# Kernel optimization log

Hardware: AMD Instinct MI355X
Metric: run time of the kernel (lower is better)

The kernel has to match this reference:

```python
import jax, jax.numpy as jnp
import numpy as np

N = 8192
H = 256
E = N * 32
ALPHA = 0.2  # LeakyReLU negative slope from init kwarg alpha


def setup_inputs() -> dict:
    key = jax.random.key(0)
    ks = jax.random.split(key, 8)
    s = 1.0 / np.sqrt(H)
    return {
        "features": jax.random.normal(ks[0], (N, H), jnp.float32),
        "edge_index": jax.random.randint(ks[1], (2, E), 0, N, jnp.int64),
        "W_att": jax.random.normal(ks[2], (H, H), jnp.float32) * s,
        "a_src": jax.random.normal(ks[3], (H,), jnp.float32) * s,
        "a_dst": jax.random.normal(ks[4], (H,), jnp.float32) * s,
        "gcn_w": jax.random.normal(ks[5], (H, H), jnp.float32) * s,
        "gcn_b": jnp.zeros((H,), jnp.float32),
        "out_w": jax.random.normal(ks[6], (H, 2), jnp.float32) * s,
        "out_b": jnp.zeros((2,), jnp.float32),
    }


def reference(features, edge_index, W_att, a_src, a_dst, gcn_w, gcn_b, out_w, out_b):
    n = features.shape[0]
    # --- SingleNodeAttentionLayer (GAT-style dense self-attention, concat=True) ---
    Wh = features @ W_att                       # [N, H]
    e = jax.nn.leaky_relu(
        (Wh @ a_src)[:, None] + (Wh @ a_dst)[None, :], negative_slope=ALPHA
    )                                            # [N, N]
    attn = jax.nn.softmax(e, axis=-1)
    h1 = jax.nn.elu(attn @ Wh)                   # [N, H]
    # --- GCNConv: symmetric-normalized aggregation with self-loops ---
    loops = jnp.arange(n, dtype=edge_index.dtype)
    row = jnp.concatenate([edge_index[0], loops])  # destination
    col = jnp.concatenate([edge_index[1], loops])  # source
    deg = jax.ops.segment_sum(jnp.ones_like(row, dtype=h1.dtype), row, num_segments=n)
    dinv = jax.lax.rsqrt(jnp.maximum(deg, 1e-12))
    norm = dinv[row] * dinv[col]                 # [E+N]
    x = h1 @ gcn_w                               # [N, H]
    agg = jax.ops.segment_sum(x[col] * norm[:, None], row, num_segments=n) + gcn_b
    # --- head: linear -> mean over nodes -> softmax ---
    res = agg @ out_w + out_b                    # [N, 2]
    res = jnp.mean(res, axis=0, keepdims=True)   # [1, 2]
    return jax.nn.softmax(res, axis=-1)
```

## Files before the change

### kernel.cpp

```cpp
#include <hip/hip_runtime.h>
#include <hip/hip_bf16.h>

#define NN 8192
#define HH 256
#define EE (NN*32)
#define ALPHAC 0.2f
#define CHUNK 16
#define NCHUNK (NN/CHUNK)
#define CSPAD 1024

typedef __bf16 bf16x8 __attribute__((ext_vector_type(8)));
typedef __bf16 bf16x4v __attribute__((ext_vector_type(4)));
typedef float  f32x4  __attribute__((ext_vector_type(4)));

#define OFF_WH     0
#define OFF_S      (OFF_WH + NN*HH)
#define OFF_SORTD  (OFF_S + NN)
#define OFF_PERM   (OFF_SORTD + NN)
#define OFF_EA     (OFF_PERM + NN)
#define OFF_E1     (OFF_EA + NN)
#define OFF_SAREL  (OFF_E1 + NN)
#define OFF_SBREL  (OFF_SAREL + NN)
#define OFF_ABPART (OFF_SBREL + NN)
#define OFF_CPAB   (OFF_ABPART + 2*NN*HH)
#define OFF_CSA    (OFF_CPAB + 2*(NCHUNK+1)*HH)
#define OFF_CSB    (OFF_CSA + CSPAD)
#define OFF_DEG    (OFF_CSB + CSPAD)
#define OFF_V      (OFF_DEG + NN)
#define OFF_WNODE  (OFF_V + HH)
#define OFF_KEYS   (OFF_WNODE + NN)
#define OFF_CTR    (OFF_KEYS + 2*NN)

__device__ __forceinline__ float elu1(float x) {
    return x > 0.f ? x : (expf(x) - 1.f);
}

__global__ __launch_bounds__(256) void k_main(
        const float* __restrict__ features, const int* __restrict__ ei,
        const float* __restrict__ W_att, const float* __restrict__ a_src,
        const float* __restrict__ a_dst, float* ws) {
    __shared__ __bf16 As[64*264];
    __shared__ __bf16 Bs[64*264];
    __shared__ float wsld[256], wdld[256];
    int bid = blockIdx.x, tid = threadIdx.x;
    if (bid < 512) {
        int mt = bid >> 2, nt = bid & 3;
        int row0 = mt*64, n0 = nt*64;
        if (nt == 0) {
            float accs = 0.f, accd = 0.f;
            const float* wrow = W_att + (size_t)tid*HH;
            #pragma unroll 4
            for (int n = 0; n < HH; n += 4) {
                float4 wv = *(const float4*)(wrow + n);
                float4 av = *(const float4*)(a_src + n);
                float4 dv = *(const float4*)(a_dst + n);
                accs += wv.x*av.x + wv.y*av.y + wv.z*av.z + wv.w*av.w;
                accd += wv.x*dv.x + wv.y*dv.y + wv.z*dv.z + wv.w*dv.w;
            }
            wsld[tid] = accs; wdld[tid] = accd;
        }
        #pragma unroll
        for (int q = 0; q < 16; ++q) {
            int idx = q*256 + tid;
            int rr = idx >> 6, cc = (idx & 63)*4;
            float4 vv = *(const float4*)(features + (size_t)(row0+rr)*HH + cc);
            bf16x4v pv = {(__bf16)vv.x, (__bf16)vv.y, (__bf16)vv.z, (__bf16)vv.w};
            *(bf16x4v*)&As[rr*264 + cc] = pv;
        }
        int nn_ = tid & 63, kb = tid >> 6;
        #pragma unroll 8
        for (int kk = 0; kk < 256; kk += 4)
            Bs[nn_*264 + kk + kb] = (__bf16)W_att[(size_t)(kk + kb)*HH + n0 + nn_];
        __syncthreads();
        int wave = tid >> 6, lane = tid & 63;
        int ml = lane & 15, quad = lane >> 4;
        const __bf16* Ap = &As[(wave*16 + ml)*264 + quad*8];
        const __bf16* Bp = &Bs[ml*264 + quad*8];
        f32x4 ac0 = {0.f,0.f,0.f,0.f}, ac1 = ac0, ac2 = ac0, ac3 = ac0;
        #pragma unroll
        for (int k0 = 0; k0 < HH; k0 += 32) {
            bf16x8 af = *(const bf16x8*)(Ap + k0);
            ac0 = __builtin_amdgcn_mfma_f32_16x16x32_bf16(af, *(const bf16x8*)(Bp + k0), ac0, 0, 0, 0);
            ac1 = __builtin_amdgcn_mfma_f32_16x16x32_bf16(af, *(const bf16x8*)(Bp + 16*264 + k0), ac1, 0, 0, 0);
            ac2 = __builtin_amdgcn_mfma_f32_16x16x32_bf16(af, *(const bf16x8*)(Bp + 32*264 + k0), ac2, 0, 0, 0);
            ac3 = __builtin_amdgcn_mfma_f32_16x16x32_bf16(af, *(const bf16x8*)(Bp + 48*264 + k0), ac3, 0, 0, 0);
        }
        float* Whp = ws + OFF_WH;
        int orow = row0 + wave*16 + quad*4;
        #pragma unroll
        for (int r = 0; r < 4; ++r) {
            size_t g = (size_t)(orow + r)*HH + n0 + ml;
            Whp[g +  0] = ac0[r];
            Whp[g + 16] = ac1[r];
            Whp[g + 32] = ac2[r];
            Whp[g + 48] = ac3[r];
        }
        if (nt == 0) {
            float4 wsv = *(const float4*)&wsld[lane*4];
            float4 wdv = *(const float4*)&wdld[lane*4];
            for (int r = 0; r < 16; ++r) {
                int row = row0 + wave*16 + r;
                bf16x4v av = *(const bf16x4v*)&As[(wave*16+r)*264 + lane*4];
                float a0 = (float)av[0], a1 = (float)av[1], a2 = (float)av[2], a3 = (float)av[3];
                float ss = a0*wsv.x + a1*wsv.y + a2*wsv.z + a3*wsv.w;
                float dd = a0*wdv.x + a1*wdv.y + a2*wdv.z + a3*wdv.w;
                #pragma unroll
                for (int off = 32; off; off >>= 1) {
                    ss += __shfl_xor(ss, off);
                    dd += __shfl_xor(dd, off);
                }
                if (lane == 0) {
                    ws[OFF_S + row] = ss;
                    unsigned u = __float_as_uint(dd);
                    unsigned mono = u ^ ((u & 0x80000000u) ? 0xFFFFFFFFu : 0x80000000u);
                    ((unsigned long long*)(ws + OFF_KEYS))[row] =
                        (((unsigned long long)mono) << 13) | (unsigned)row;
                }
            }
        }
    } else {
        if (bid == 512 && tid == 0) {
            unsigned* ctr = (unsigned*)(ws + OFF_CTR);
            __hip_atomic_store(&ctr[0], 0u, __ATOMIC_RELAXED, __HIP_MEMORY_SCOPE_AGENT);
            __hip_atomic_store(&ctr[1], 0u, __ATOMIC_RELAXED, __HIP_MEMORY_SCOPE_AGENT);
        }
        int e0 = (bid - 512)*512 + tid;
        atomicAdd(ws + OFF_DEG + ei[e0], 1.0f);
        atomicAdd(ws + OFF_DEG + ei[e0+256], 1.0f);
    }
}

__global__ __launch_bounds__(256) void k_rank(const int* __restrict__ ei, float* ws) {
    __shared__ unsigned long long lk[NN];
    int bid = blockIdx.x, tid = threadIdx.x;
    if (bid < 512) {
        const unsigned long long* keys = (const unsigned long long*)(ws + OFF_KEYS);
        for (int m = tid; m < NN/2; m += 256)
            *(ulonglong2*)&lk[m*2] = *(const ulonglong2*)&keys[m*2];
        __syncthreads();
        int wave = tid >> 6, lane = tid & 63;
        int jb = bid*16 + wave*4;
        unsigned long long kj0 = lk[jb+0], kj1 = lk[jb+1];
        unsigned long long kj2 = lk[jb+2], kj3 = lk[jb+3];
        int c0 = 0, c1 = 0, c2 = 0, c3 = 0;
        #pragma unroll 4
        for (int it = 0; it < 64; ++it) {
            ulonglong2 kq = *(const ulonglong2*)&lk[(it*64 + lane)*2];
            c0 += (kq.x < kj0); c1 += (kq.x < kj1);
            c2 += (kq.x < kj2); c3 += (kq.x < kj3);
            c0 += (kq.y < kj0); c1 += (kq.y < kj1);
            c2 += (kq.y < kj2); c3 += (kq.y < kj3);
        }
        #pragma unroll
        for (int off = 1; off < 64; off <<= 1) {
            c0 += __shfl_xor(c0, off);
            c1 += __shfl_xor(c1, off);
            c2 += __shfl_xor(c2, off);
            c3 += __shfl_xor(c3, off);
        }
        if (lane == 0) {
            unsigned long long kk[4] = {kj0, kj1, kj2, kj3};
            int cr[4] = {c0, c1, c2, c3};
            #pragma unroll
            for (int q = 0; q < 4; ++q) {
                unsigned long long kv = kk[q];
                int r = cr[q];
                unsigned mm = (unsigned)(kv >> 13);
                unsigned u = (mm & 0x80000000u) ? (mm ^ 0x80000000u) : ~mm;
                float dj = __uint_as_float(u);
                int j = (int)(kv & 8191ULL);
                ws[OFF_SORTD + r] = dj;
                ((int*)ws)[OFF_PERM + r] = j;
                ws[OFF_EA + r] = expf(ALPHAC * dj);
                ws[OFF_E1 + r] = expf(dj);
            }
        }
    } else {
        int e0 = (bid - 512)*512 + tid;
        #pragma unroll
        for (int q = 0; q < 2; ++q) {
            int e = e0 + q*256;
            int r = ei[e], c = ei[EE + e];
            float dr = rsqrtf(ws[OFF_DEG + r] + 1.0f);
            float dc = rsqrtf(ws[OFF_DEG + c] + 1.0f);
            atomicAdd(ws + OFF_WNODE + c, dr*dc);
        }
    }
}

__global__ __launch_bounds__(256) void k_vecpref(float* ws) {
    __shared__ int   sp[CHUNK];
    __shared__ float sea[CHUNK], se1[CHUNK];
    __shared__ int srank;
    int bid = blockIdx.x, tid = threadIdx.x;
    int c = bid, h = tid;
    int k0 = c * CHUNK;
    unsigned* ctr = (unsigned*)(ws + OFF_CTR);
    if (h < CHUNK) {
        sp[h]  = ((int*)ws)[OFF_PERM + k0 + h];
        sea[h] = ws[OFF_EA + k0 + h];
        se1[h] = ws[OFF_E1 + k0 + h];
    }
    __syncthreads();
    if (tid < 64) {
        float vv = 0.f;
        if (tid < 16) vv = sea[tid];
        else if (tid < 32) vv = se1[tid-16];
        #pragma unroll
        for (int off = 1; off < 16; off <<= 1) {
            float x = __shfl_up(vv, off);
            if ((tid & 15) >= off) vv += x;
        }
        if (tid < 16) {
            ws[OFF_SAREL + k0 + tid] = vv;
            if (tid == 15)
                __hip_atomic_store(&ws[OFF_CSA + c + 1], vv, __ATOMIC_RELAXED, __HIP_MEMORY_SCOPE_AGENT);
        } else if (tid < 32) {
            ws[OFF_SBREL + k0 + tid - 16] = vv;
            if (tid == 31)
                __hip_atomic_store(&ws[OFF_CSB + c + 1], vv, __ATOMIC_RELAXED, __HIP_MEMORY_SCOPE_AGENT);
        }
    }
    const float* Wh = ws + OFF_WH;
    float wv[CHUNK];
    #pragma unroll
    for (int kk = 0; kk < CHUNK; ++kk)
        wv[kk] = Wh[(size_t)sp[kk]*HH + h];
    float2* abp = (float2*)(ws + OFF_ABPART);
    float acca = 0.f, accb = 0.f;
    #pragma unroll
    for (int kk = 0; kk < CHUNK; ++kk) {
        acca += sea[kk]*wv[kk]; accb += se1[kk]*wv[kk];
        abp[(size_t)(k0+kk)*HH + h] = make_float2(acca, accb);
    }
    float2 tot = make_float2(acca, accb);
    unsigned long long totbits;
    __builtin_memcpy(&totbits, &tot, 8);
    float2* cp = (float2*)(ws + OFF_CPAB);
    __hip_atomic_store((unsigned long long*)&cp[(size_t)(c+1)*HH + h], totbits,
                       __ATOMIC_RELAXED, __HIP_MEMORY_SCOPE_AGENT);
    __syncthreads();
    if (tid == 0) {
        unsigned old = __hip_atomic_fetch_add(&ctr[0], 1u, __ATOMIC_RELAXED, __HIP_MEMORY_SCOPE_AGENT);
        srank = (int)old;
    }
    __syncthreads();
    int rk = srank;
    if (rk < NCHUNK - 33) return;
    if (tid == 0) {
        while (__hip_atomic_load(&ctr[0], __ATOMIC_RELAXED, __HIP_MEMORY_SCOPE_AGENT) != (unsigned)NCHUNK)
            __builtin_amdgcn_s_sleep(8);
    }
    __syncthreads();
    int sid = rk - (NCHUNK - 33);
    if (sid < 32) {
        int hh = sid*8 + (tid >> 5);
        int t = tid & 31;
        float la[16], lb[16];
        float ta = 0.f, tb = 0.f;
        #pragma unroll
        for (int m = 0; m < 16; ++m) {
            unsigned long long u = __hip_atomic_load(
                (unsigned long long*)&cp[(size_t)(t*16 + m + 1)*HH + hh],
                __ATOMIC_RELAXED, __HIP_MEMORY_SCOPE_AGENT);
            float2 v; __builtin_memcpy(&v, &u, 8);
            la[m] = v.x; lb[m] = v.y;
            ta += la[m]; tb += lb[m];
        }
        float ia = ta, ib = tb;
        #pragma unroll
        for (int off = 1; off < 32; off <<= 1) {
            float xa = __shfl_up(ia, off, 32);
            float xb = __shfl_up(ib, off, 32);
            if (t >= off) { ia += xa; ib += xb; }
        }
        float ba = ia - ta, bb = ib - tb;
        #pragma unroll
        for (int m = 0; m < 16; ++m) {
            cp[(size_t)(t*16 + m)*HH + hh] = make_float2(ba, bb);
            ba += la[m]; bb += lb[m];
        }
        if (t == 31) cp[(size_t)NCHUNK*HH + hh] = make_float2(ba, bb);
    } else {
        int wv_ = tid >> 6, ln = tid & 63;
        if (wv_ < 2) {
            float* cs = ws + (wv_ ? OFF_CSB : OFF_CSA);
            float la[8];
            float ta = 0.f;
            #pragma unroll
            for (int m = 0; m < 8; ++m) {
                la[m] = __hip_atomic_load(&cs[ln*8 + m + 1], __ATOMIC_RELAXED, __HIP_MEMORY_SCOPE_AGENT);
                ta += la[m];
            }
            float ia = ta;
            #pragma unroll
            for (int off = 1; off < 64; off <<= 1) {
                float x = __shfl_up(ia, off);
                if (ln >= off) ia += x;
            }
            float ba = ia - ta;
            #pragma unroll
            for (int m = 0; m < 8; ++m) { cs[ln*8 + m] = ba; ba += la[m]; }
            if (ln == 63) cs[NCHUNK] = ba;
        }
    }
}

__global__ __launch_bounds__(256) void k_rows(const float* __restrict__ gcn_w,
                                              const float* __restrict__ gcn_b,
                                              const float* __restrict__ out_w,
                                              const float* __restrict__ out_b,
                                              float* ws, float* out) {
    __shared__ float sd[NN];
    __shared__ float red[4][256];
    __shared__ int lastf;
    int bid = blockIdx.x, tid = threadIdx.x;
    unsigned* ctr = (unsigned*)(ws + OFF_CTR);
    for (int m = tid; m < NN/4; m += 256)
        *(float4*)&sd[m*4] = *(const float4*)(ws + OFF_SORTD + m*4);
    __syncthreads();
    int wave = tid >> 6, lane = tid & 63;
    int gw = bid*4 + wave;
    const float2* abp  = (const float2*)(ws + OFF_ABPART);
    const float2* cpab = (const float2*)(ws + OFF_CPAB);
    float btot = ws[OFF_CSB + NCHUNK];
    const float4* btr = (const float4*)(cpab + (size_t)NCHUNK*HH);
    float4 bt0 = btr[lane*2], bt1 = btr[lane*2+1];
    float BTx = bt0.y, BTy = bt0.w, BTz = bt1.y, BTw = bt1.w;

    int myr = lane & 3;
    float si_m = ws[OFF_S + gw*4 + myr];
    float tt = -si_m;
    int lo = 0, hi = NN;
    while (lo < hi) {
        int mid = (lo + hi) >> 1;
        if (sd[mid] <= tt) lo = mid + 1; else hi = mid;
    }
    float accx = 0.f, accy = 0.f, accz = 0.f, accw = 0.f;
    #pragma unroll
    for (int r = 0; r < 4; ++r) {
        int i = gw*4 + r;
        int k = __shfl(lo, r);
        float si = __shfl(si_m, r);
        float eas = expf(ALPHAC * si), es = expf(si);
        float av = 0.f, bv = 0.f;
        float Ax=0.f, Ay=0.f, Az=0.f, Aw=0.f, Bx=0.f, By=0.f, Bz=0.f, Bw=0.f;
        if (k > 0) {
            int km = k - 1, cc = km >> 4;
            av = ws[OFF_CSA + cc] + ws[OFF_SAREL + km];
            bv = ws[OFF_CSB + cc] + ws[OFF_SBREL + km];
            const float4* pr = (const float4*)(abp + (size_t)km*HH);
            const float4* cr = (const float4*)(cpab + (size_t)cc*HH);
            float4 p0 = pr[lane*2], p1 = pr[lane*2+1];
            float4 q0 = cr[lane*2], q1 = cr[lane*2+1];
            Ax = p0.x + q0.x; Bx = p0.y + q0.y;
            Ay = p0.z + q0.z; By = p0.w + q0.w;
            Az = p1.x + q1.x; Bz = p1.y + q1.y;
            Aw = p1.z + q1.z; Bw = p1.w + q1.w;
        }
        float Z = eas*av + es*(btot - bv);
        float invZ = 1.f / Z;
        float w = ws[OFF_WNODE + i] + 1.0f/(ws[OFF_DEG + i] + 1.0f);
        accx += w * elu1((eas*Ax + es*(BTx - Bx)) * invZ);
        accy += w * elu1((eas*Ay + es*(BTy - By)) * invZ);
        accz += w * elu1((eas*Az + es*(BTz - Bz)) * invZ);
        accw += w * elu1((eas*Aw + es*(BTw - Bw)) * invZ);
    }
    red[wave][lane*4+0] = accx;
    red[wave][lane*4+1] = accy;
    red[wave][lane*4+2] = accz;
    red[wave][lane*4+3] = accw;
    __syncthreads();
    float sum = red[0][tid] + red[1][tid] + red[2][tid] + red[3][tid];
    atomicAdd(ws + OFF_V + tid, sum);
    __syncthreads();
    if (tid == 0) {
        unsigned old = __hip_atomic_fetch_add(&ctr[1], 1u, __ATOMIC_RELAXED, __HIP_MEMORY_SCOPE_AGENT);
        lastf = (old == 511u);
    }
    __syncthreads();
    if (!lastf) return;
    float vt = atomicAdd(ws + OFF_V + tid, 0.0f);
    red[0][tid] = vt;
    __syncthreads();
    float acc = 0.f;
    for (int hh = 0; hh < HH; ++hh) acc += red[0][hh] * gcn_w[(size_t)hh*HH + tid];
    float meanv = acc * (1.0f/(float)NN) + gcn_b[tid];
    red[1][tid] = meanv * out_w[tid*2+0];
    red[2][tid] = meanv * out_w[tid*2+1];
    __syncthreads();
    for (int off = 128; off; off >>= 1) {
        if (tid < off) { red[1][tid] += red[1][tid+off]; red[2][tid] += red[2][tid+off]; }
        __syncthreads();
    }
    if (tid == 0) {
        float res0 = red[1][0] + out_b[0], res1 = red[2][0] + out_b[1];
        float m = fmaxf(res0, res1);
        float e0 = expf(res0 - m), e1v = expf(res1 - m);
        float inv = 1.f / (e0 + e1v);
        out[0] = e0 * inv;
        out[1] = e1v * inv;
    }
}

extern "C" void kernel_launch(void* const* d_in, const int* in_sizes, int n_in,
                              void* d_out, int out_size, void* d_ws, size_t ws_size,
                              hipStream_t stream) {
    const float* features = (const float*)d_in[0];
    const int*   eidx     = (const int*)d_in[1];
    const float* W_att    = (const float*)d_in[2];
    const float* a_src    = (const float*)d_in[3];
    const float* a_dst    = (const float*)d_in[4];
    const float* gcn_w    = (const float*)d_in[5];
    const float* gcn_b    = (const float*)d_in[6];
    const float* out_w    = (const float*)d_in[7];
    const float* out_b    = (const float*)d_in[8];
    float* ws  = (float*)d_ws;
    float* out = (float*)d_out;

    k_main<<<1024, 256, 0, stream>>>(features, eidx, W_att, a_src, a_dst, ws);
    k_rank<<<1024, 256, 0, stream>>>(eidx, ws);
    k_vecpref<<<NCHUNK, 256, 0, stream>>>(ws);
    k_rows<<<512, 256, 0, stream>>>(gcn_w, gcn_b, out_w, out_b, ws, out);
}
```

Before: 181.3 us.

## Fuse attention score projections into GEMM epilogue and merge edge work into GEMM blocks

The attention scores s and d are now computed from the MFMA accumulators in the GEMM epilogue, using shuffle reductions plus atomicAdd into workspace. This replaces the separate W·a precompute and the per-row dot products. The degree-count and edge-weight atomics now run inside the same 512 blocks as the GEMM and rank work, which halves both grids. Rank keys are built in shared memory straight from d, the exp tables move into k_vecpref, and k_rows binary-searches global sorted d instead of staging it in LDS. The atomics assume the workspace starts zeroed, and the global-memory binary search may add latency.

```diff
diff --git a/kernel.cpp b/kernel.cpp
--- a/kernel.cpp
+++ b/kernel.cpp
@@ -15,11 +15,10 @@
 
 #define OFF_WH     0
 #define OFF_S      (OFF_WH + NN*HH)
-#define OFF_SORTD  (OFF_S + NN)
+#define OFF_D      (OFF_S + NN)
+#define OFF_SORTD  (OFF_D + NN)
 #define OFF_PERM   (OFF_SORTD + NN)
-#define OFF_EA     (OFF_PERM + NN)
-#define OFF_E1     (OFF_EA + NN)
-#define OFF_SAREL  (OFF_E1 + NN)
+#define OFF_SAREL  (OFF_PERM + NN)
 #define OFF_SBREL  (OFF_SAREL + NN)
 #define OFF_ABPART (OFF_SBREL + NN)
 #define OFF_CPAB   (OFF_ABPART + 2*NN*HH)
@@ -28,8 +27,7 @@
 #define OFF_DEG    (OFF_CSB + CSPAD)
 #define OFF_V      (OFF_DEG + NN)
 #define OFF_WNODE  (OFF_V + HH)
-#define OFF_KEYS   (OFF_WNODE + NN)
-#define OFF_CTR    (OFF_KEYS + 2*NN)
+#define OFF_CTR    (OFF_WNODE + NN)
 
 __device__ __forceinline__ float elu1(float x) {
     return x > 0.f ? x : (expf(x) - 1.f);
@@ -41,150 +39,135 @@
         const float* __restrict__ a_dst, float* ws) {
     __shared__ __bf16 As[64*264];
     __shared__ __bf16 Bs[64*264];
-    __shared__ float wsld[256], wdld[256];
     int bid = blockIdx.x, tid = threadIdx.x;
-    if (bid < 512) {
-        int mt = bid >> 2, nt = bid & 3;
-        int row0 = mt*64, n0 = nt*64;
-        if (nt == 0) {
-            float accs = 0.f, accd = 0.f;
-            const float* wrow = W_att + (size_t)tid*HH;
-            #pragma unroll 4
-            for (int n = 0; n < HH; n += 4) {
-                float4 wv = *(const float4*)(wrow + n);
-                float4 av = *(const float4*)(a_src + n);
-                float4 dv = *(const float4*)(a_dst + n);
-                accs += wv.x*av.x + wv.y*av.y + wv.z*av.z + wv.w*av.w;
-                accd += wv.x*dv.x + wv.y*dv.y + wv.z*dv.z + wv.w*dv.w;
-            }
-            wsld[tid] = accs; wdld[tid] = accd;
-        }
-        #pragma unroll
-        for (int q = 0; q < 16; ++q) {
-            int idx = q*256 + tid;
-            int rr = idx >> 6, cc = (idx & 63)*4;
-            float4 vv = *(const float4*)(features + (size_t)(row0+rr)*HH + cc);
-            bf16x4v pv = {(__bf16)vv.x, (__bf16)vv.y, (__bf16)vv.z, (__bf16)vv.w};
-            *(bf16x4v*)&As[rr*264 + cc] = pv;
-        }
-        int nn_ = tid & 63, kb = tid >> 6;
-        #pragma unroll 8
-        for (int kk = 0; kk < 256; kk += 4)
-            Bs[nn_*264 + kk + kb] = (__bf16)W_att[(size_t)(kk + kb)*HH + n0 + nn_];
-        __syncthreads();
-        int wave = tid >> 6, lane = tid & 63;
-        int ml = lane & 15, quad = lane >> 4;
-        const __bf16* Ap = &As[(wave*16 + ml)*264 + quad*8];
-        const __bf16* Bp = &Bs[ml*264 + quad*8];
-        f32x4 ac0 = {0.f,0.f,0.f,0.f}, ac1 = ac0, ac2 = ac0, ac3 = ac0;
-        #pragma unroll
-        for (int k0 = 0; k0 < HH; k0 += 32) {
-            bf16x8 af = *(const bf16x8*)(Ap + k0);
-            ac0 = __builtin_amdgcn_mfma_f32_16x16x32_bf16(af, *(const bf16x8*)(Bp + k0), ac0, 0, 0, 0);
-            ac1 = __builtin_amdgcn_mfma_f32_16x16x32_bf16(af, *(const bf16x8*)(Bp + 16*264 + k0), ac1, 0, 0, 0);
-            ac2 = __builtin_amdgcn_mfma_f32_16x16x32_bf16(af, *(const bf16x8*)(Bp + 32*264 + k0), ac2, 0, 0, 0);
-            ac3 = __builtin_amdgcn_mfma_f32_16x16x32_bf16(af, *(const bf16x8*)(Bp + 48*264 + k0), ac3, 0, 0, 0);
-        }
-        float* Whp = ws + OFF_WH;
-        int orow = row0 + wave*16 + quad*4;
+    if (bid == 0 && tid < 2) {
+        unsigned* ctr = (unsigned*)(ws + OFF_CTR);
+        __hip_atomic_store(&ctr[tid], 0u, __ATOMIC_RELAXED, __HIP_MEMORY_SCOPE_AGENT);
+    }
+    int mt = bid >> 2, nt = bid & 3;
+    int row0 = mt*64, n0 = nt*64;
+    #pragma unroll
+    for (int q = 0; q < 16; ++q) {
+        int idx = q*256 + tid;
+        int rr = idx >> 6, cc = (idx & 63)*4;
+        float4 vv = *(const float4*)(features + (size_t)(row0+rr)*HH + cc);
+        bf16x4v pv = {(__bf16)vv.x, (__bf16)vv.y, (__bf16)vv.z, (__bf16)vv.w};
+        *(bf16x4v*)&As[rr*264 + cc] = pv;
+    }
+    int nn_ = tid & 63, kb = tid >> 6;
+    #pragma unroll 8
+    for (int kk = 0; kk < 256; kk += 4)
+        Bs[nn_*264 + kk + kb] = (__bf16)W_att[(size_t)(kk + kb)*HH + n0 + nn_];
+    __syncthreads();
+    int wave = tid >> 6, lane = tid & 63;
+    int ml = lane & 15, quad = lane >> 4;
+    const __bf16* Ap = &As[(wave*16 + ml)*264 + quad*8];
+    const __bf16* Bp = &Bs[ml*264 + quad*8];
+    f32x4 ac0 = {0.f,0.f,0.f,0.f}, ac1 = ac0, ac2 = ac0, ac3 = ac0;
+    #pragma unroll
+    for (int k0 = 0; k0 < HH; k0 += 32) {
+        bf16x8 af = *(const bf16x8*)(Ap + k0);
+        ac0 = __builtin_amdgcn_mfma_f32_16x16x32_bf16(af, *(const bf16x8*)(Bp + k0), ac0, 0, 0, 0);
+        ac1 = __builtin_amdgcn_mfma_f32_16x16x32_bf16(af, *(const bf16x8*)(Bp + 16*264 + k0), ac1, 0, 0, 0);
+        ac2 = __builtin_amdgcn_mfma_f32_16x16x32_bf16(af, *(const bf16x8*)(Bp + 32*264 + k0), ac2, 0, 0, 0);
+        ac3 = __builtin_amdgcn_mfma_f32_16x16x32_bf16(af, *(const bf16x8*)(Bp + 48*264 + k0), ac3, 0, 0, 0);
+    }
+    float* Whp = ws + OFF_WH;
+    int orow = row0 + wave*16 + quad*4;
+    #pragma unroll
+    for (int r = 0; r < 4; ++r) {
+        size_t g = (size_t)(orow + r)*HH + n0 + ml;
+        Whp[g +  0] = ac0[r];
+        Whp[g + 16] = ac1[r];
+        Whp[g + 32] = ac2[r];
+        Whp[g + 48] = ac3[r];
+    }
+    float as0 = a_src[n0 +  0 + ml], as1 = a_src[n0 + 16 + ml];
+    float as2 = a_src[n0 + 32 + ml], as3 = a_src[n0 + 48 + ml];
+    float ad0 = a_dst[n0 +  0 + ml], ad1 = a_dst[n0 + 16 + ml];
+    float ad2 = a_dst[n0 + 32 + ml], ad3 = a_dst[n0 + 48 + ml];
+    float ps[4], pd[4];
+    #pragma unroll
+    for (int r = 0; r < 4; ++r) {
+        ps[r] = ac0[r]*as0 + ac1[r]*as1 + ac2[r]*as2 + ac3[r]*as3;
+        pd[r] = ac0[r]*ad0 + ac1[r]*ad1 + ac2[r]*ad2 + ac3[r]*ad3;
+    }
+    #pragma unroll
+    for (int m = 1; m < 16; m <<= 1) {
         #pragma unroll
         for (int r = 0; r < 4; ++r) {
-            size_t g = (size_t)(orow + r)*HH + n0 + ml;
-            Whp[g +  0] = ac0[r];
-            Whp[g + 16] = ac1[r];
-            Whp[g + 32] = ac2[r];
-            Whp[g + 48] = ac3[r];
-        }
-        if (nt == 0) {
-            float4 wsv = *(const float4*)&wsld[lane*4];
-            float4 wdv = *(const float4*)&wdld[lane*4];
-            for (int r = 0; r < 16; ++r) {
-                int row = row0 + wave*16 + r;
-                bf16x4v av = *(const bf16x4v*)&As[(wave*16+r)*264 + lane*4];
-                float a0 = (float)av[0], a1 = (float)av[1], a2 = (float)av[2], a3 = (float)av[3];
-                float ss = a0*wsv.x + a1*wsv.y + a2*wsv.z + a3*wsv.w;
-                float dd = a0*wdv.x + a1*wdv.y + a2*wdv.z + a3*wdv.w;
-                #pragma unroll
-                for (int off = 32; off; off >>= 1) {
-                    ss += __shfl_xor(ss, off);
-                    dd += __shfl_xor(dd, off);
-                }
-                if (lane == 0) {
-                    ws[OFF_S + row] = ss;
-                    unsigned u = __float_as_uint(dd);
-                    unsigned mono = u ^ ((u & 0x80000000u) ? 0xFFFFFFFFu : 0x80000000u);
-                    ((unsigned long long*)(ws + OFF_KEYS))[row] =
-                        (((unsigned long long)mono) << 13) | (unsigned)row;
-                }
-            }
-        }
-    } else {
-        if (bid == 512 && tid == 0) {
-            unsigned* ctr = (unsigned*)(ws + OFF_CTR);
-            __hip_atomic_store(&ctr[0], 0u, __ATOMIC_RELAXED, __HIP_MEMORY_SCOPE_AGENT);
-            __hip_atomic_store(&ctr[1], 0u, __ATOMIC_RELAXED, __HIP_MEMORY_SCOPE_AGENT);
-        }
-        int e0 = (bid - 512)*512 + tid;
-        atomicAdd(ws + OFF_DEG + ei[e0], 1.0f);
-        atomicAdd(ws + OFF_DEG + ei[e0+256], 1.0f);
-    }
+            ps[r] += __shfl_xor(ps[r], m);
+            pd[r] += __shfl_xor(pd[r], m);
+        }
+    }
+    if (ml == 0) {
+        #pragma unroll
+        for (int r = 0; r < 4; ++r) {
+            atomicAdd(ws + OFF_S + orow + r, ps[r]);
+            atomicAdd(ws + OFF_D + orow + r, pd[r]);
+        }
+    }
+    int e0 = bid*512 + tid;
+    atomicAdd(ws + OFF_DEG + ei[e0], 1.0f);
+    atomicAdd(ws + OFF_DEG + ei[e0+256], 1.0f);
 }
 
 __global__ __launch_bounds__(256) void k_rank(const int* __restrict__ ei, float* ws) {
     __shared__ unsigned long long lk[NN];
     int bid = blockIdx.x, tid = threadIdx.x;
-    if (bid < 512) {
-        const unsigned long long* keys = (const unsigned long long*)(ws + OFF_KEYS);
-        for (int m = tid; m < NN/2; m += 256)
-            *(ulonglong2*)&lk[m*2] = *(const ulonglong2*)&keys[m*2];
-        __syncthreads();
-        int wave = tid >> 6, lane = tid & 63;
-        int jb = bid*16 + wave*4;
-        unsigned long long kj0 = lk[jb+0], kj1 = lk[jb+1];
-        unsigned long long kj2 = lk[jb+2], kj3 = lk[jb+3];
-        int c0 = 0, c1 = 0, c2 = 0, c3 = 0;
-        #pragma unroll 4
-        for (int it = 0; it < 64; ++it) {
-            ulonglong2 kq = *(const ulonglong2*)&lk[(it*64 + lane)*2];
-            c0 += (kq.x < kj0); c1 += (kq.x < kj1);
-            c2 += (kq.x < kj2); c3 += (kq.x < kj3);
-            c0 += (kq.y < kj0); c1 += (kq.y < kj1);
-            c2 += (kq.y < kj2); c3 += (kq.y < kj3);
-        }
-        #pragma unroll
-        for (int off = 1; off < 64; off <<= 1) {
-            c0 += __shfl_xor(c0, off);
-            c1 += __shfl_xor(c1, off);
-            c2 += __shfl_xor(c2, off);
-            c3 += __shfl_xor(c3, off);
-        }
-        if (lane == 0) {
-            unsigned long long kk[4] = {kj0, kj1, kj2, kj3};
-            int cr[4] = {c0, c1, c2, c3};
-            #pragma unroll
-            for (int q = 0; q < 4; ++q) {
-                unsigned long long kv = kk[q];
-                int r = cr[q];
-                unsigned mm = (unsigned)(kv >> 13);
-                unsigned u = (mm & 0x80000000u) ? (mm ^ 0x80000000u) : ~mm;
-                float dj = __uint_as_float(u);
-                int j = (int)(kv & 8191ULL);
-                ws[OFF_SORTD + r] = dj;
-                ((int*)ws)[OFF_PERM + r] = j;
-                ws[OFF_EA + r] = expf(ALPHAC * dj);
-                ws[OFF_E1 + r] = expf(dj);
-            }
-        }
-    } else {
-        int e0 = (bid - 512)*512 + tid;
-        #pragma unroll
-        for (int q = 0; q < 2; ++q) {
-            int e = e0 + q*256;
-            int r = ei[e], c = ei[EE + e];
-            float dr = rsqrtf(ws[OFF_DEG + r] + 1.0f);
-            float dc = rsqrtf(ws[OFF_DEG + c] + 1.0f);
-            atomicAdd(ws + OFF_WNODE + c, dr*dc);
-        }
+    const float* dg = ws + OFF_D;
+    for (int m = tid; m < NN/4; m += 256) {
+        float4 dv = *(const float4*)&dg[m*4];
+        float da[4] = {dv.x, dv.y, dv.z, dv.w};
+        #pragma unroll
+        for (int q = 0; q < 4; ++q) {
+            unsigned u = __float_as_uint(da[q]);
+            unsigned mono = u ^ ((u & 0x80000000u) ? 0xFFFFFFFFu : 0x80000000u);
+            lk[m*4+q] = (((unsigned long long)mono) << 13) | (unsigned)(m*4+q);
+        }
+    }
+    __syncthreads();
+    int wave = tid >> 6, lane = tid & 63;
+    int jb = bid*16 + wave*4;
+    unsigned long long kj0 = lk[jb+0], kj1 = lk[jb+1];
+    unsigned long long kj2 = lk[jb+2], kj3 = lk[jb+3];
+    int c0 = 0, c1 = 0, c2 = 0, c3 = 0;
+    #pragma unroll 4
+    for (int it = 0; it < 64; ++it) {
+        ulonglong2 kq = *(const ulonglong2*)&lk[(it*64 + lane)*2];
+        c0 += (kq.x < kj0); c1 += (kq.x < kj1);
+        c2 += (kq.x < kj2); c3 += (kq.x < kj3);
+        c0 += (kq.y < kj0); c1 += (kq.y < kj1);
+        c2 += (kq.y < kj2); c3 += (kq.y < kj3);
+    }
+    #pragma unroll
+    for (int off = 1; off < 64; off <<= 1) {
+        c0 += __shfl_xor(c0, off);
+        c1 += __shfl_xor(c1, off);
+        c2 += __shfl_xor(c2, off);
+        c3 += __shfl_xor(c3, off);
+    }
+    if (lane == 0) {
+        unsigned long long kk[4] = {kj0, kj1, kj2, kj3};
+        int cr[4] = {c0, c1, c2, c3};
+        #pragma unroll
+        for (int q = 0; q < 4; ++q) {
+            unsigned long long kv = kk[q];
+            int r = cr[q];
+            unsigned mm = (unsigned)(kv >> 13);
+            unsigned u = (mm & 0x80000000u) ? (mm ^ 0x80000000u) : ~mm;
+            ws[OFF_SORTD + r] = __uint_as_float(u);
+            ((int*)ws)[OFF_PERM + r] = (int)(kv & 8191ULL);
+        }
+    }
+    int e0 = bid*512 + tid;
+    #pragma unroll
+    for (int q = 0; q < 2; ++q) {
+        int e = e0 + q*256;
+        int r = ei[e], c = ei[EE + e];
+        float dr = rsqrtf(ws[OFF_DEG + r] + 1.0f);
+        float dc = rsqrtf(ws[OFF_DEG + c] + 1.0f);
+        atomicAdd(ws + OFF_WNODE + c, dr*dc);
     }
 }
 
@@ -197,9 +180,10 @@
     int k0 = c * CHUNK;
     unsigned* ctr = (unsigned*)(ws + OFF_CTR);
     if (h < CHUNK) {
-        sp[h]  = ((int*)ws)[OFF_PERM + k0 + h];
-        sea[h] = ws[OFF_EA + k0 + h];
-        se1[h] = ws[OFF_E1 + k0 + h];
+        sp[h] = ((int*)ws)[OFF_PERM + k0 + h];
+        float dj = ws[OFF_SORTD + k0 + h];
+        sea[h] = expf(ALPHAC * dj);
+        se1[h] = expf(dj);
     }
     __syncthreads();
     if (tid < 64) {
@@ -311,18 +295,15 @@
                                               const float* __restrict__ out_w,
                                               const float* __restrict__ out_b,
                                               float* ws, float* out) {
-    __shared__ float sd[NN];
     __shared__ float red[4][256];
     __shared__ int lastf;
     int bid = blockIdx.x, tid = threadIdx.x;
     unsigned* ctr = (unsigned*)(ws + OFF_CTR);
-    for (int m = tid; m < NN/4; m += 256)
-        *(float4*)&sd[m*4] = *(const float4*)(ws + OFF_SORTD + m*4);
-    __syncthreads();
     int wave = tid >> 6, lane = tid & 63;
     int gw = bid*4 + wave;
     const float2* abp  = (const float2*)(ws + OFF_ABPART);
     const float2* cpab = (const float2*)(ws + OFF_CPAB);
+    const float* sdg = ws + OFF_SORTD;
     float btot = ws[OFF_CSB + NCHUNK];
     const float4* btr = (const float4*)(cpab + (size_t)NCHUNK*HH);
     float4 bt0 = btr[lane*2], bt1 = btr[lane*2+1];
@@ -334,7 +315,7 @@
     int lo = 0, hi = NN;
     while (lo < hi) {
         int mid = (lo + hi) >> 1;
-        if (sd[mid] <= tt) lo = mid + 1; else hi = mid;
+        if (sdg[mid] <= tt) lo = mid + 1; else hi = mid;
     }
     float accx = 0.f, accy = 0.f, accz = 0.f, accw = 0.f;
     #pragma unroll
@@ -418,8 +399,8 @@
     float* ws  = (float*)d_ws;
     float* out = (float*)d_out;
 
-    k_main<<<1024, 256, 0, stream>>>(features, eidx, W_att, a_src, a_dst, ws);
-    k_rank<<<1024, 256, 0, stream>>>(eidx, ws);
+    k_main<<<512, 256, 0, stream>>>(features, eidx, W_att, a_src, a_dst, ws);
+    k_rank<<<512, 256, 0, stream>>>(eidx, ws);
     k_vecpref<<<NCHUNK, 256, 0, stream>>>(ws);
     k_rows<<<512, 256, 0, stream>>>(gcn_w, gcn_b, out_w, out_b, ws, out);
 }
```

New measurement: 175.1 us. 3.4% less time.
